# Kernel tuning notes

Hardware: AMD Instinct MI355X
Metric: run time of the kernel (lower is better)

The kernel has to match this reference:

```python
import jax, jax.numpy as jnp
import numpy as np

# Dims: C = 8*8*4 = 256 input channels, O = 8*8*8 = 512 output channels,
# space_rank = 4, TT ranks = (4, 16, 16).

def setup_inputs() -> dict:
    key = jax.random.key(0)
    ks = jax.random.split(key, 6)
    inp = jax.random.normal(ks[0], (32, 256, 32, 32), dtype=jnp.float32)
    # space_factor: (space_rank, 1, kH, kW)
    space_factor = jax.random.normal(ks[1], (4, 1, 3, 3), dtype=jnp.float32) * 0.3
    # factors[i]: (in_i, rank_i, rank_{i+1}, out_i)
    factor0 = jax.random.normal(ks[2], (8, 4, 16, 8), dtype=jnp.float32) * 0.1
    factor1 = jax.random.normal(ks[3], (8, 16, 16, 8), dtype=jnp.float32) * 0.08
    # last_factor: (in_last, rank_last, out_last)
    last_factor = jax.random.normal(ks[4], (4, 16, 8), dtype=jnp.float32) * 0.1
    bias = jax.random.uniform(ks[5], (512,), dtype=jnp.float32, minval=-0.02, maxval=0.02)
    return {"input": inp, "space_factor": space_factor, "factor0": factor0,
            "factor1": factor1, "last_factor": last_factor, "bias": bias}


def reference(input, space_factor, factor0, factor1, last_factor, bias):
    B, C, H, W = input.shape
    sr = space_factor.shape[0]
    # Depthwise conv: each of the C channels convolved with the same
    # `space_rank` filters (torch repeat along out-channel dim + groups=C).
    w = jnp.tile(space_factor, (C, 1, 1, 1))  # (C*sr, 1, kH, kW)
    y = jax.lax.conv_general_dilated(
        input, w, window_strides=(1, 1), padding=[(1, 1), (1, 1)],
        feature_group_count=C,
        dimension_numbers=("NCHW", "OIHW", "NCHW"))  # (B, C*sr, H', W')
    Hp, Wp = y.shape[2], y.shape[3]
    # (B, n0, n1, n2, sr, H', W') with (n0,n1,n2) = input_chanel_shape
    t = y.reshape(B, 8, 8, 4, sr, Hp, Wp)
    # Contract the tiny TT cores first (optimal order found by tn.contractors.optimal):
    # chain: (n0, n1, n2, r0, o0, o1, o2) -- only ~0.5M elements.
    chain = jnp.einsum("apqx,bqry,crz->abcpxyz", factor0, factor1, last_factor)
    # One big contraction over (n0, n1, n2, r0): effectively a GEMM
    # (B*H'*W', C*sr) x (C*sr, O).
    out = jnp.einsum("nabcphw,abcpxyz->nxyzhw", t, chain)
    out = out.reshape(B, 512, Hp, Wp)
    return out + bias[None, :, None, None]
```

## Files before the change

kernel.cpp:

```cpp
#include <hip/hip_runtime.h>

typedef unsigned short ushort_t;
typedef __attribute__((ext_vector_type(8))) short bf16x8;
typedef __attribute__((ext_vector_type(8))) unsigned short ushort8;
typedef __attribute__((ext_vector_type(4))) float f32x4;

__device__ __forceinline__ unsigned short f2bf(float f) {
  union { float f; unsigned u; } x; x.f = f;
  unsigned r = x.u + 0x7FFFu + ((x.u >> 16) & 1u);
  return (unsigned short)(r >> 16);
}

__global__ void chain_g_kernel(const float* __restrict__ f1,
                               const float* __restrict__ lf,
                               float* __restrict__ g) {
  int idx = blockIdx.x * 256 + threadIdx.x;
  int z = idx & 7, c = (idx >> 3) & 3, y = (idx >> 5) & 7,
      q = (idx >> 8) & 15, b = idx >> 12;
  float s = 0.f;
  #pragma unroll
  for (int r = 0; r < 16; ++r)
    s += f1[((b * 16 + q) * 16 + r) * 8 + y] * lf[(c * 16 + r) * 8 + z];
  g[idx] = s;
}

__global__ void chain_kernel(const float* __restrict__ f0,
                             const float* __restrict__ g,
                             ushort_t* __restrict__ chainT) {
  int idx = blockIdx.x * 256 + threadIdx.x;
  int k = idx & 1023, o = idx >> 10;
  int p = k & 3, c = (k >> 2) & 3, b = (k >> 4) & 7, a = k >> 7;
  int z = o & 7, y = (o >> 3) & 7, x = o >> 6;
  float s = 0.f;
  #pragma unroll
  for (int q = 0; q < 16; ++q)
    s += f0[((a * 4 + p) * 16 + q) * 8 + x] *
         g[(((b * 16 + q) * 8 + y) * 4 + c) * 8 + z];
  chainT[idx] = f2bf(s);
}

__global__ __launch_bounds__(256) void conv_kernel(const float* __restrict__ in,
                                                   const float* __restrict__ sf,
                                                   ushort_t* __restrict__ t) {
  __shared__ float in_lds[64][164];
  __shared__ float sf_l[36];
  int bid = blockIdx.x;
  int cq = bid & 3, h2 = (bid >> 2) & 15, n = bid >> 6;
  int h0 = h2 * 2;
  int tid = threadIdx.x;
  if (tid < 36) sf_l[tid] = sf[tid];
  { int ch = tid >> 2, r = tid & 3;
    in_lds[ch][r * 40 + 3] = 0.f;
    in_lds[ch][r * 40 + 36] = 0.f; }
  const float* inb = in + ((size_t)n * 256 + cq * 64) * 1024;
  #pragma unroll
  for (int i = 0; i < 8; ++i) {
    int e = tid + i * 256;
    int ch = e >> 5, rem = e & 31;
    int r = rem >> 3, w4 = rem & 7;
    int hh = h0 - 1 + r;
    float4 v = make_float4(0.f, 0.f, 0.f, 0.f);
    if (hh >= 0 && hh < 32)
      v = *(const float4*)&inb[(size_t)ch * 1024 + hh * 32 + w4 * 4];
    *(float4*)&in_lds[ch][r * 40 + 4 + w4 * 4] = v;
  }
  __syncthreads();
  float sfr[36];
  #pragma unroll
  for (int i = 0; i < 36; ++i) sfr[i] = sf_l[i];
  int w = tid >> 3, gg = tid & 7;
  size_t m0 = (size_t)n * 1024 + (size_t)h0 * 32 + w;
  #pragma unroll
  for (int j = 0; j < 4; ++j) {
    float acc[2][2][4];
    #pragma unroll
    for (int b = 0; b < 2; ++b) {
      int ch = j * 16 + gg * 2 + b;
      float vals[4][3];
      #pragma unroll
      for (int r = 0; r < 4; ++r)
        #pragma unroll
        for (int dw = 0; dw < 3; ++dw)
          vals[r][dw] = in_lds[ch][r * 40 + 3 + w + dw];
      #pragma unroll
      for (int hh = 0; hh < 2; ++hh)
        #pragma unroll
        for (int p = 0; p < 4; ++p) {
          float s = 0.f;
          #pragma unroll
          for (int dr = 0; dr < 3; ++dr)
            #pragma unroll
            for (int dw = 0; dw < 3; ++dw)
              s += vals[hh + dr][dw] * sfr[p * 9 + dr * 3 + dw];
          acc[hh][b][p] = s;
        }
    }
    #pragma unroll
    for (int hh = 0; hh < 2; ++hh) {
      ushort8 outv;
      #pragma unroll
      for (int b = 0; b < 2; ++b)
        #pragma unroll
        for (int p = 0; p < 4; ++p) outv[b * 4 + p] = f2bf(acc[hh][b][p]);
      *(ushort8*)&t[(m0 + hh * 32) * 1024 + (size_t)(cq * 256 + j * 64 + gg * 8)] = outv;
    }
  }
}

#define AS1 __attribute__((address_space(1)))
#define AS3 __attribute__((address_space(3)))
#define BARRIER __builtin_amdgcn_s_barrier()
#define SBAR    __builtin_amdgcn_sched_barrier(0)
#define VMCNT4  asm volatile("s_waitcnt vmcnt(4)" ::: "memory")
#define VMCNT0  asm volatile("s_waitcnt vmcnt(0)" ::: "memory")

__global__ __launch_bounds__(512, 2) void gemm_kernel(const ushort_t* __restrict__ tA,
                                                      const ushort_t* __restrict__ tB,
                                                      const float* __restrict__ bias,
                                                      float* __restrict__ out) {
  __shared__ __align__(16) ushort_t smem[65536];
  int tid = threadIdx.x;
  int bid = blockIdx.x;
  int wg = (bid & 7) * 32 + (bid >> 3);
  int tile_m = (wg >> 1) * 256;
  int tile_n = (wg & 1) * 256;

  int lane = tid & 63, wv = tid >> 6;
  int wm2 = wv >> 2, wn4 = wv & 3;
  int lr = lane & 15, kg = lane >> 4;
  int kph0 = ((kg * 8) ^ ((lane & 7) * 8));
  int kph1 = ((32 + kg * 8) ^ ((lane & 7) * 8));
  int arow = wm2 * 128 + lr;
  int brow = wn4 * 64 + lr;

  int srow = tid >> 3;
  int scol = ((tid & 7) ^ (srow & 7)) * 8;
  const ushort_t* sA = tA + (size_t)(tile_m + srow) * 1024 + scol;
  const ushort_t* sB = tB + (size_t)(tile_n + srow) * 1024 + scol;

#define STAGE_A(buf, koff, h)                                                                  \
  __builtin_amdgcn_global_load_lds((const AS1 void*)(sA + (size_t)((h)*128) * 1024 + (koff)),  \
      (AS3 void*)&smem[(buf)*16384 + (h)*8192 + tid*8], 16, 0, 0);                             \
  __builtin_amdgcn_global_load_lds((const AS1 void*)(sA + (size_t)((h)*128+64) * 1024 + (koff)),\
      (AS3 void*)&smem[(buf)*16384 + (h)*8192 + 4096 + tid*8], 16, 0, 0);
#define STAGE_B(buf, koff, h)                                                                  \
  __builtin_amdgcn_global_load_lds((const AS1 void*)(sB + (size_t)((h)*128) * 1024 + (koff)),  \
      (AS3 void*)&smem[32768 + (buf)*16384 + (h)*8192 + tid*8], 16, 0, 0);                     \
  __builtin_amdgcn_global_load_lds((const AS1 void*)(sB + (size_t)((h)*128+64) * 1024 + (koff)),\
      (AS3 void*)&smem[32768 + (buf)*16384 + (h)*8192 + 4096 + tid*8], 16, 0, 0);

#define READ_A(dst, mbase, buf)                                                                \
  _Pragma("unroll")                                                                            \
  for (int mf = 0; mf < 4; ++mf) {                                                             \
    dst[mf][0] = *(const bf16x8*)&smem[(buf)*16384 + (arow + (mbase) + mf*16)*64 + kph0];      \
    dst[mf][1] = *(const bf16x8*)&smem[(buf)*16384 + (arow + (mbase) + mf*16)*64 + kph1];      \
  }
#define READ_B(dst, nbase, buf)                                                                \
  _Pragma("unroll")                                                                            \
  for (int nf = 0; nf < 2; ++nf) {                                                             \
    dst[nf][0] = *(const bf16x8*)&smem[32768 + (buf)*16384 + (brow + (nbase) + nf*16)*64 + kph0];\
    dst[nf][1] = *(const bf16x8*)&smem[32768 + (buf)*16384 + (brow + (nbase) + nf*16)*64 + kph1];\
  }
#define Q_MFMA(AF, BF, MB, NB)                                                                 \
  __builtin_amdgcn_s_setprio(1);                                                              \
  _Pragma("unroll")                                                                            \
  for (int mf = 0; mf < 4; ++mf)                                                               \
    _Pragma("unroll")                                                                          \
    for (int nf = 0; nf < 2; ++nf)                                                             \
      _Pragma("unroll")                                                                        \
      for (int ks = 0; ks < 2; ++ks)                                                           \
        acc[(MB) + mf][(NB) + nf] = __builtin_amdgcn_mfma_f32_16x16x32_bf16(                   \
            AF[mf][ks], BF[nf][ks], acc[(MB) + mf][(NB) + nf], 0, 0, 0);                       \
  __builtin_amdgcn_s_setprio(0);

  f32x4 acc[8][4];
  #pragma unroll
  for (int i = 0; i < 8; ++i)
    #pragma unroll
    for (int j = 0; j < 4; ++j) acc[i][j] = (f32x4){0.f, 0.f, 0.f, 0.f};

  bf16x8 a1[4][2], a2[4][2], b1[2][2], b2[2][2];

  STAGE_A(0, 0, 0) STAGE_A(0, 0, 1) STAGE_B(0, 0, 0) STAGE_B(0, 0, 1)
  STAGE_A(1, 64, 0) STAGE_A(1, 64, 1)
  VMCNT0; BARRIER;

#define ITER(I_, FULL)                                                                         \
  {                                                                                            \
    int k1 = (2*(I_)+1)*64, k2 = (2*(I_)+2)*64, k3 = (2*(I_)+3)*64;                            \
                                                                 \
    VMCNT4; SBAR;                                                                              \
    READ_A(a1, 0, 0) READ_B(b1, 0, 0)                                                          \
    STAGE_B(1, k1, 0) SBAR; BARRIER; SBAR;                                                     \
    Q_MFMA(a1, b1, 0, 0) SBAR; BARRIER;                                                        \
                                                                                       \
    READ_B(b2, 32, 0) STAGE_B(1, k1, 1) SBAR; BARRIER; SBAR;                                   \
    Q_MFMA(a1, b2, 0, 2) SBAR; BARRIER;                                                        \
                                                                                       \
    READ_A(a2, 64, 0) if (FULL) { STAGE_A(0, k2, 0) } SBAR; BARRIER; SBAR;                     \
    Q_MFMA(a2, b2, 4, 2) SBAR; BARRIER;                                                        \
                                                                                       \
    if (FULL) { STAGE_A(0, k2, 1) } SBAR; BARRIER; SBAR;                                       \
    Q_MFMA(a2, b1, 4, 0) SBAR; BARRIER;                                                        \
                                                                  \
    if (FULL) { VMCNT4; } else { VMCNT0; } SBAR;                                               \
    READ_A(a1, 0, 1) READ_B(b1, 0, 1)                                                          \
    if (FULL) { STAGE_B(0, k2, 0) } SBAR; BARRIER; SBAR;                                       \
    Q_MFMA(a1, b1, 0, 0) SBAR; BARRIER;                                                        \
                                                                                       \
    READ_B(b2, 32, 1) if (FULL) { STAGE_B(0, k2, 1) } SBAR; BARRIER; SBAR;                     \
    Q_MFMA(a1, b2, 0, 2) SBAR; BARRIER;                                                        \
                                                                                       \
    READ_A(a2, 64, 1) if (FULL) { STAGE_A(1, k3, 0) } SBAR; BARRIER; SBAR;                     \
    Q_MFMA(a2, b2, 4, 2) SBAR; BARRIER;                                                        \
                                                                                       \
    if (FULL) { STAGE_A(1, k3, 1) } SBAR; BARRIER; SBAR;                                       \
    Q_MFMA(a2, b1, 4, 0) SBAR; BARRIER;                                                        \
  }

  for (int I = 0; I < 7; ++I) ITER(I, 1)
  ITER(7, 0)
#undef ITER

  #pragma unroll
  for (int mf = 0; mf < 8; ++mf)
    #pragma unroll
    for (int nf = 0; nf < 4; ++nf) {
      int m = tile_m + wm2 * 128 + mf * 16 + kg * 4;
      int o = tile_n + wn4 * 64 + nf * 16 + lr;
      float bv = bias[o];
      f32x4 v = acc[mf][nf];
      v[0] += bv; v[1] += bv; v[2] += bv; v[3] += bv;
      *(f32x4*)&out[(size_t)(m >> 10) * 524288 + (size_t)o * 1024 + (size_t)(m & 1023)] = v;
    }
}

extern "C" void kernel_launch(void* const* d_in, const int* in_sizes, int n_in,
                              void* d_out, int out_size, void* d_ws, size_t ws_size,
                              hipStream_t stream) {
  (void)in_sizes; (void)n_in; (void)out_size; (void)ws_size;
  const float* in   = (const float*)d_in[0];
  const float* sf   = (const float*)d_in[1];
  const float* f0   = (const float*)d_in[2];
  const float* f1   = (const float*)d_in[3];
  const float* lf   = (const float*)d_in[4];
  const float* bias = (const float*)d_in[5];
  float* out = (float*)d_out;

  char* ws = (char*)d_ws;
  ushort_t* t      = (ushort_t*)ws;
  ushort_t* chainT = (ushort_t*)(ws + 67108864);
  float*    g      = (float*)(ws + 67108864 + 1048576);

  hipLaunchKernelGGL(chain_g_kernel, dim3(128),  dim3(256), 0, stream, f1, lf, g);
  hipLaunchKernelGGL(chain_kernel,   dim3(2048), dim3(256), 0, stream, f0, g, chainT);
  hipLaunchKernelGGL(conv_kernel,    dim3(2048), dim3(256), 0, stream, in, sf, t);
  hipLaunchKernelGGL(gemm_kernel,    dim3(256),  dim3(512), 0, stream, t, chainT, bias, out);
}
```

Measured before the change: 77.90 us.

## Enlarge conv row tile, drop GEMM sched barriers, relax prologue wait

The depthwise conv kernel now computes four output rows per block instead of two, loading a 6-row halo. This halves the grid and cuts redundant halo loads. In the GEMM, all sched_barrier fences are removed so the compiler can interleave LDS reads, global stages and MFMAs more freely. The prologue also waits with vmcnt(4) instead of vmcnt(0), which risks reading the second A stage before it has landed, and the freer schedule may reorder the hand-tuned interleaving badly.

```diff
diff --git a/kernel.cpp b/kernel.cpp
--- a/kernel.cpp
+++ b/kernel.cpp
@@ -42,21 +42,23 @@
 __global__ __launch_bounds__(256) void conv_kernel(const float* __restrict__ in,
                                                    const float* __restrict__ sf,
                                                    ushort_t* __restrict__ t) {
-  __shared__ float in_lds[64][164];
+  __shared__ float in_lds[64][244];
   __shared__ float sf_l[36];
   int bid = blockIdx.x;
-  int cq = bid & 3, h2 = (bid >> 2) & 15, n = bid >> 6;
-  int h0 = h2 * 2;
+  int cq = bid & 3, h4 = (bid >> 2) & 7, n = bid >> 5;
+  int h0 = h4 * 4;
   int tid = threadIdx.x;
   if (tid < 36) sf_l[tid] = sf[tid];
-  { int ch = tid >> 2, r = tid & 3;
+  for (int e = tid; e < 384; e += 256) {
+    int ch = e / 6, r = e % 6;
     in_lds[ch][r * 40 + 3] = 0.f;
-    in_lds[ch][r * 40 + 36] = 0.f; }
+    in_lds[ch][r * 40 + 36] = 0.f;
+  }
   const float* inb = in + ((size_t)n * 256 + cq * 64) * 1024;
   #pragma unroll
-  for (int i = 0; i < 8; ++i) {
+  for (int i = 0; i < 12; ++i) {
     int e = tid + i * 256;
-    int ch = e >> 5, rem = e & 31;
+    int ch = e / 48, rem = e % 48;
     int r = rem >> 3, w4 = rem & 7;
     int hh = h0 - 1 + r;
     float4 v = make_float4(0.f, 0.f, 0.f, 0.f);
@@ -72,18 +74,18 @@
   size_t m0 = (size_t)n * 1024 + (size_t)h0 * 32 + w;
   #pragma unroll
   for (int j = 0; j < 4; ++j) {
-    float acc[2][2][4];
+    float acc[4][2][4];
     #pragma unroll
     for (int b = 0; b < 2; ++b) {
       int ch = j * 16 + gg * 2 + b;
-      float vals[4][3];
+      float vals[6][3];
       #pragma unroll
-      for (int r = 0; r < 4; ++r)
+      for (int r = 0; r < 6; ++r)
         #pragma unroll
         for (int dw = 0; dw < 3; ++dw)
           vals[r][dw] = in_lds[ch][r * 40 + 3 + w + dw];
       #pragma unroll
-      for (int hh = 0; hh < 2; ++hh)
+      for (int hh = 0; hh < 4; ++hh)
         #pragma unroll
         for (int p = 0; p < 4; ++p) {
           float s = 0.f;
@@ -96,7 +98,7 @@
         }
     }
     #pragma unroll
-    for (int hh = 0; hh < 2; ++hh) {
+    for (int hh = 0; hh < 4; ++hh) {
       ushort8 outv;
       #pragma unroll
       for (int b = 0; b < 2; ++b)
@@ -110,7 +112,6 @@
 #define AS1 __attribute__((address_space(1)))
 #define AS3 __attribute__((address_space(3)))
 #define BARRIER __builtin_amdgcn_s_barrier()
-#define SBAR    __builtin_amdgcn_sched_barrier(0)
 #define VMCNT4  asm volatile("s_waitcnt vmcnt(4)" ::: "memory")
 #define VMCNT0  asm volatile("s_waitcnt vmcnt(0)" ::: "memory")
 
@@ -183,39 +184,39 @@
 
   STAGE_A(0, 0, 0) STAGE_A(0, 0, 1) STAGE_B(0, 0, 0) STAGE_B(0, 0, 1)
   STAGE_A(1, 64, 0) STAGE_A(1, 64, 1)
-  VMCNT0; BARRIER;
+  VMCNT4; BARRIER;
 
 #define ITER(I_, FULL)                                                                         \
   {                                                                                            \
     int k1 = (2*(I_)+1)*64, k2 = (2*(I_)+2)*64, k3 = (2*(I_)+3)*64;                            \
                                                                  \
-    VMCNT4; SBAR;                                                                              \
+    VMCNT4;                                                                                    \
     READ_A(a1, 0, 0) READ_B(b1, 0, 0)                                                          \
-    STAGE_B(1, k1, 0) SBAR; BARRIER; SBAR;                                                     \
-    Q_MFMA(a1, b1, 0, 0) SBAR; BARRIER;                                                        \
-                                                                                       \
-    READ_B(b2, 32, 0) STAGE_B(1, k1, 1) SBAR; BARRIER; SBAR;                                   \
-    Q_MFMA(a1, b2, 0, 2) SBAR; BARRIER;                                                        \
-                                                                                       \
-    READ_A(a2, 64, 0) if (FULL) { STAGE_A(0, k2, 0) } SBAR; BARRIER; SBAR;                     \
-    Q_MFMA(a2, b2, 4, 2) SBAR; BARRIER;                                                        \
-                                                                                       \
-    if (FULL) { STAGE_A(0, k2, 1) } SBAR; BARRIER; SBAR;                                       \
-    Q_MFMA(a2, b1, 4, 0) SBAR; BARRIER;                                                        \
+    STAGE_B(1, k1, 0) BARRIER;                                                                 \
+    Q_MFMA(a1, b1, 0, 0) BARRIER;                                                              \
+                                                                                       \
+    READ_B(b2, 32, 0) STAGE_B(1, k1, 1) BARRIER;                                               \
+    Q_MFMA(a1, b2, 0, 2) BARRIER;                                                              \
+                                                                                       \
+    READ_A(a2, 64, 0) if (FULL) { STAGE_A(0, k2, 0) } BARRIER;                                 \
+    Q_MFMA(a2, b2, 4, 2) BARRIER;                                                              \
+                                                                                       \
+    if (FULL) { STAGE_A(0, k2, 1) } BARRIER;                                                   \
+    Q_MFMA(a2, b1, 4, 0) BARRIER;                                                              \
                                                                   \
-    if (FULL) { VMCNT4; } else { VMCNT0; } SBAR;                                               \
+    if (FULL) { VMCNT4; } else { VMCNT0; }                                                     \
     READ_A(a1, 0, 1) READ_B(b1, 0, 1)                                                          \
-    if (FULL) { STAGE_B(0, k2, 0) } SBAR; BARRIER; SBAR;                                       \
-    Q_MFMA(a1, b1, 0, 0) SBAR; BARRIER;                                                        \
-                                                                                       \
-    READ_B(b2, 32, 1) if (FULL) { STAGE_B(0, k2, 1) } SBAR; BARRIER; SBAR;                     \
-    Q_MFMA(a1, b2, 0, 2) SBAR; BARRIER;                                                        \
-                                                                                       \
-    READ_A(a2, 64, 1) if (FULL) { STAGE_A(1, k3, 0) } SBAR; BARRIER; SBAR;                     \
-    Q_MFMA(a2, b2, 4, 2) SBAR; BARRIER;                                                        \
-                                                                                       \
-    if (FULL) { STAGE_A(1, k3, 1) } SBAR; BARRIER; SBAR;                                       \
-    Q_MFMA(a2, b1, 4, 0) SBAR; BARRIER;                                                        \
+    if (FULL) { STAGE_B(0, k2, 0) } BARRIER;                                                   \
+    Q_MFMA(a1, b1, 0, 0) BARRIER;                                                              \
+                                                                                       \
+    READ_B(b2, 32, 1) if (FULL) { STAGE_B(0, k2, 1) } BARRIER;                                 \
+    Q_MFMA(a1, b2, 0, 2) BARRIER;                                                              \
+                                                                                       \
+    READ_A(a2, 64, 1) if (FULL) { STAGE_A(1, k3, 0) } BARRIER;                                 \
+    Q_MFMA(a2, b2, 4, 2) BARRIER;                                                              \
+                                                                                       \
+    if (FULL) { STAGE_A(1, k3, 1) } BARRIER;                                                   \
+    Q_MFMA(a2, b1, 4, 0) BARRIER;                                                              \
   }
 
   for (int I = 0; I < 7; ++I) ITER(I, 1)
@@ -254,6 +255,6 @@
 
   hipLaunchKernelGGL(chain_g_kernel, dim3(128),  dim3(256), 0, stream, f1, lf, g);
   hipLaunchKernelGGL(chain_kernel,   dim3(2048), dim3(256), 0, stream, f0, g, chainT);
-  hipLaunchKernelGGL(conv_kernel,    dim3(2048), dim3(256), 0, stream, in, sf, t);
+  hipLaunchKernelGGL(conv_kernel,    dim3(1024), dim3(256), 0, stream, in, sf, t);
   hipLaunchKernelGGL(gemm_kernel,    dim3(256),  dim3(512), 0, stream, t, chainT, bias, out);
 }
```

After: 75.39 us. -3.2%, faster.
